# Kernel optimization log

Measured on AMD Instinct MI355X. Metric: run time of the kernel, lower is better.

## Reference

```python
import jax, jax.numpy as jnp
import numpy as np

EPS_IN = 1e-5   # InstanceNorm eps
EPS_L1 = 1e-12  # F.normalize eps


def conv1x1(x, w, b):
    # x: [B,C,H,W], w: [O,C], b: [O]
    return jnp.einsum('bchw,oc->bohw', x, w) + b[None, :, None, None]


def conv3x3_reflect(x, w, b):
    xp = jnp.pad(x, ((0, 0), (0, 0), (1, 1), (1, 1)), mode='reflect')
    y = jax.lax.conv_general_dilated(xp, w, (1, 1), 'VALID',
                                     dimension_numbers=('NCHW', 'OIHW', 'NCHW'))
    return y + b[None, :, None, None]


def instance_norm(x):
    mu = x.mean(axis=(2, 3), keepdims=True)
    var = x.var(axis=(2, 3), keepdims=True)  # biased, matches torch InstanceNorm
    return (x - mu) * jax.lax.rsqrt(var + EPS_IN)


def res_block(x, w1, b1, w2, b2):
    h = jax.nn.relu(instance_norm(conv3x3_reflect(x, w1, b1)))
    h = instance_norm(conv3x3_reflect(h, w2, b2))
    return x + h


def _nearest_idx(out_size, in_size):
    # torch F.interpolate(mode='nearest'): src = floor(dst * in/out)
    return (np.arange(out_size) * in_size) // out_size


def forward(x, mask, g_w, g_b, theta_w, theta_b, phi_w, phi_b, W_w, W_b,
            res_w1, res_b1, res_w2, res_b2):
    B, C, H, Wd = x.shape
    N = H * Wd
    g_x = conv1x1(x, g_w, g_b).reshape(B, -1, N).transpose(0, 2, 1)      # [B,N,Ci]
    theta_x = conv1x1(x, theta_w, theta_b).reshape(B, -1, N).transpose(0, 2, 1)
    phi_x = conv1x1(x, phi_w, phi_b).reshape(B, -1, N)                   # [B,Ci,N]
    f = jnp.einsum('bnc,bcm->bnm', theta_x, phi_x)  # temperature = 1.0
    f_div_C = jax.nn.softmax(f, axis=2)
    # mask pipeline
    m = jax.image.resize(mask, (B, 1, H, Wd), method='linear')  # bilinear, half-pixel (align_corners=False)
    m = jnp.where(m > 0, 1.0, m)
    m = 1.0 - m
    hi = _nearest_idx(H, mask.shape[2])
    wi = _nearest_idx(Wd, mask.shape[3])
    tmp = (1.0 - mask)[:, :, hi][:, :, :, wi]  # nearest upsample of (1-mask)
    m = m * tmp                                 # [B,1,H,W]
    f_div_C = f_div_C * m.reshape(B, 1, N)      # broadcast instead of N^2 repeat
    # re_norm=True: L1 renormalize along keys
    f_div_C = f_div_C / jnp.maximum(jnp.sum(jnp.abs(f_div_C), axis=2, keepdims=True), EPS_L1)
    y = jnp.einsum('bnm,bmc->bnc', f_div_C, g_x)             # [B,N,Ci]
    y = y.transpose(0, 2, 1).reshape(B, -1, H, Wd)
    W_y = conv1x1(y, W_w, W_b)
    for i in range(3):
        W_y = res_block(W_y, res_w1[i], res_b1[i], res_w2[i], res_b2[i])
    z = m * x + (1.0 - m) * W_y
    return z


def setup_inputs() -> dict:
    key = jax.random.key(0)
    ks = jax.random.split(key, 16)
    B, C, H, W = 4, 256, 64, 64
    x = jax.random.normal(ks[0], (B, C, H, W), dtype=jnp.float32)
    mask = (jax.random.uniform(ks[1], (B, 1, 32, 32)) < 0.5).astype(jnp.float32)
    s = 0.02
    d = {
        'x': x, 'mask': mask,
        'g_w': jax.random.normal(ks[2], (C, C), jnp.float32) * s,
        'g_b': jnp.zeros((C,), jnp.float32),
        'theta_w': jax.random.normal(ks[3], (C, C), jnp.float32) * s,
        'theta_b': jnp.zeros((C,), jnp.float32),
        'phi_w': jax.random.normal(ks[4], (C, C), jnp.float32) * s,
        'phi_b': jnp.zeros((C,), jnp.float32),
        'W_w': jax.random.normal(ks[5], (C, C), jnp.float32) * s,
        'W_b': jnp.zeros((C,), jnp.float32),
        'res_w1': jax.random.normal(ks[6], (3, C, C, 3, 3), jnp.float32) * s,
        'res_b1': jnp.zeros((3, C), jnp.float32),
        'res_w2': jax.random.normal(ks[7], (3, C, C, 3, 3), jnp.float32) * s,
        'res_b2': jnp.zeros((3, C), jnp.float32),
    }
    return d


def reference(x, mask, g_w, g_b, theta_w, theta_b, phi_w, phi_b, W_w, W_b,
              res_w1, res_b1, res_w2, res_b2):
    return forward(x, mask, g_w, g_b, theta_w, theta_b, phi_w, phi_b, W_w, W_b,
                   res_w1, res_b1, res_w2, res_b2)
```

## Files before the change

### kernel.cpp

```cpp
#include <hip/hip_runtime.h>

#define BB   4
#define CC   256
#define NPIX 4096
#define PB   1048576
#define NTOT 16384

typedef __attribute__((ext_vector_type(8))) short bf16x8;
typedef __attribute__((ext_vector_type(4))) float f32x4;
typedef __attribute__((ext_vector_type(4))) unsigned short u16x4;

__device__ __forceinline__ unsigned short f2b(float f) {
  union { float f; unsigned u; } v; v.f = f;
  unsigned r = v.u + 0x7fffu + ((v.u >> 16) & 1u);
  return (unsigned short)(r >> 16);
}
__device__ __forceinline__ float b2f(unsigned short h) {
  union { unsigned u; float f; } v; v.u = ((unsigned)h) << 16;
  return v.f;
}
__device__ __forceinline__ f32x4 mfma16(bf16x8 a, bf16x8 b, f32x4 c) {
  return __builtin_amdgcn_mfma_f32_16x16x32_bf16(a, b, c, 0, 0, 0);
}
__device__ __forceinline__ void gload_lds16(const unsigned short* g, unsigned short* l) {
  __builtin_amdgcn_global_load_lds(
      (const __attribute__((address_space(1))) unsigned int*)g,
      (__attribute__((address_space(3))) unsigned int*)l, 16, 0, 0);
}
__device__ __forceinline__ int remap_px(int n, int dh, int dw) {
  int h = (n >> 6) + dh;
  int w = (n & 63) + dw;
  h = h < 0 ? 1 : (h > 63 ? 62 : h);
  w = w < 0 ? 1 : (w > 63 ? 62 : w);
  return (h << 6) | w;
}

__global__ void repack_w1x1_k(const float* __restrict__ tw, const float* __restrict__ pw,
                              const float* __restrict__ gw, const float* __restrict__ Ww,
                              unsigned short* __restrict__ dst) {
  int i = blockIdx.x * 256 + threadIdx.x;
  dst[i]           = f2b(tw[i]);
  dst[65536 + i]   = f2b(pw[i]);
  dst[131072 + i]  = f2b(gw[i]);
  dst[196608 + i]  = f2b(Ww[i]);
}

__global__ void repack_bias_k(const float* __restrict__ tb, const float* __restrict__ pb,
                              const float* __restrict__ gb, const float* __restrict__ Wb,
                              float* __restrict__ bias) {
  int i = blockIdx.x * 256 + threadIdx.x;
  float v;
  if (i < 256) v = tb[i];
  else if (i < 512) v = pb[i - 256];
  else if (i < 768) v = gb[i - 512];
  else v = Wb[i - 768];
  bias[i] = v;
}

__global__ void repack_res_k(const float* __restrict__ w1, const float* __restrict__ w2,
                             unsigned short* __restrict__ wk) {
  int idx = blockIdx.x * 256 + threadIdx.x;
  if (idx >= 1769472) return;
  int t = idx % 9;
  int rest = idx / 9;
  int c = rest & 255;
  int o = (rest >> 8) & 255;
  int i = rest >> 16;
  size_t d = (size_t)t * 65536 + o * 256 + c;
  wk[(size_t)(2 * i)     * 589824 + d] = f2b(w1[idx]);
  wk[(size_t)(2 * i + 1) * 589824 + d] = f2b(w2[idx]);
}

__global__ void prep_mask_k(const float* __restrict__ mask, float* __restrict__ m) {
  int idx = blockIdx.x * 256 + threadIdx.x;
  if (idx >= BB * NPIX) return;
  int b = idx >> 12, n = idx & 4095;
  int h = n >> 6, w = n & 63;
  const float* M = mask + b * 1024;
  float sh = 0.5f * h - 0.25f, sw = 0.5f * w - 0.25f;
  int h0 = (int)floorf(sh), w0 = (int)floorf(sw);
  float th = sh - h0, tw = sw - w0;
  int h0c = min(max(h0, 0), 31), h1c = min(max(h0 + 1, 0), 31);
  int w0c = min(max(w0, 0), 31), w1c = min(max(w0 + 1, 0), 31);
  float v = (1.f - th) * ((1.f - tw) * M[h0c * 32 + w0c] + tw * M[h0c * 32 + w1c])
          +        th  * ((1.f - tw) * M[h1c * 32 + w0c] + tw * M[h1c * 32 + w1c]);
  float inv = v > 0.f ? 0.f : 1.f;
  float tmp = 1.f - M[(h >> 1) * 32 + (w >> 1)];
  m[idx] = inv * tmp;
}

__global__ void mask_scan_k(const float* __restrict__ mbuf, int* __restrict__ ci,
                            int* __restrict__ kcount) {
  int b = blockIdx.x;
  int tid = threadIdx.x;
  __shared__ int sc[256];
  const float* mb = mbuf + b * 4096;
  int n0 = tid * 16, cnt = 0;
  float mv[16];
  #pragma unroll
  for (int i = 0; i < 16; ++i) { mv[i] = mb[n0 + i]; cnt += mv[i] > 0.f ? 1 : 0; }
  sc[tid] = cnt;
  __syncthreads();
  for (int off = 1; off < 256; off <<= 1) {
    int v = sc[tid];
    int u = tid >= off ? sc[tid - off] : 0;
    __syncthreads();
    sc[tid] = v + u;
    __syncthreads();
  }
  int base = sc[tid] - cnt;
  int* cib = ci + b * 4096;
  #pragma unroll
  for (int i = 0; i < 16; ++i)
    if (mv[i] > 0.f) cib[base++] = n0 + i;
  if (tid == 255) kcount[b] = sc[255];
}

__global__ void gather_phi_k(const unsigned short* __restrict__ phb, const int* __restrict__ ci,
                             const int* __restrict__ kcount, unsigned short* __restrict__ phic) {
  int b = blockIdx.y;
  int Kb = kcount[b];
  int pad = (Kb + 63) & ~63;
  int j = blockIdx.x * 8 + (threadIdx.x >> 5);
  int cl = threadIdx.x & 31;
  if (j >= pad) return;
  bf16x8 v;
  if (j < Kb) {
    v = *(const bf16x8*)(phb + (size_t)b * PB + (size_t)ci[b * 4096 + j] * 256 + cl * 8);
  } else {
    for (int t = 0; t < 8; ++t) v[t] = 0;
  }
  *(bf16x8*)(phic + (size_t)b * PB + (size_t)j * 256 + cl * 8) = v;
}

__global__ void gather_g_k(const unsigned short* __restrict__ gbuf, const int* __restrict__ ci,
                           const int* __restrict__ kcount, unsigned short* __restrict__ gc) {
  int b = blockIdx.z;
  int Kb = kcount[b];
  int pad = (Kb + 63) & ~63;
  int c = blockIdx.y;
  int j = blockIdx.x * 256 + threadIdx.x;
  if (j >= pad) return;
  unsigned short v = 0;
  if (j < Kb) v = gbuf[(size_t)c * NTOT + b * 4096 + ci[b * 4096 + j]];
  gc[(size_t)c * NTOT + b * 4096 + j] = v;
}

__global__ void transpose_x_k(const float* __restrict__ x, unsigned short* __restrict__ xT) {
  __shared__ float T[64][65];
  int b = blockIdx.z;
  int n0 = blockIdx.x * 64, c0 = blockIdx.y * 64;
  int tx = threadIdx.x, ty = threadIdx.y;
  const float* xb = x + (size_t)b * PB;
  #pragma unroll
  for (int i = 0; i < 16; ++i) {
    int cl = ty + i * 4;
    T[cl][tx] = xb[(size_t)(c0 + cl) * NPIX + n0 + tx];
  }
  __syncthreads();
  unsigned short* ob = xT + (size_t)b * PB;
  #pragma unroll
  for (int i = 0; i < 16; ++i) {
    int nl = ty + i * 4;
    ob[(size_t)(n0 + nl) * CC + c0 + tx] = f2b(T[tx][nl]);
  }
}

template <int EPI, int TAPS>
__launch_bounds__(256, 2)
__global__ void gemm_w(const unsigned short* __restrict__ A,
                       const unsigned short* __restrict__ Bact,
                       const float* __restrict__ bias,
                       float* __restrict__ outF,
                       unsigned short* __restrict__ o0,
                       unsigned short* __restrict__ o1,
                       unsigned short* __restrict__ o2) {
  int m0 = blockIdx.y * 128;
  int bxs = (blockIdx.x & 7) * 32 + (blockIdx.x >> 3);
  int n0 = bxs * 64;
  int tid = threadIdx.x, lane = tid & 63, wid = tid >> 6;
  int wm = wid >> 1, wn = wid & 1;
  int r16 = lane & 15, g4 = lane >> 4;
  __shared__ __align__(16) unsigned short As[8192];
  __shared__ __align__(16) unsigned short Bs[4096];
  f32x4 acc[4][2] = {};
  int srow[4], scolel[4];
  #pragma unroll
  for (int i = 0; i < 4; ++i) {
    int L = tid * 16 + i * 4096;
    int row = L >> 7;
    srow[i] = row;
    scolel[i] = ((L & 127) ^ ((row & 7) << 4)) >> 1;
  }
  int ra[4], qa[4];
  #pragma unroll
  for (int i = 0; i < 4; ++i) { int r = wm * 64 + i * 16 + r16; ra[i] = r * 128; qa[i] = r & 7; }
  int rbb[2], qb[2];
  #pragma unroll
  for (int j = 0; j < 2; ++j) { int c = wn * 32 + j * 16 + r16; rbb[j] = c * 128; qb[j] = c & 7; }

  const int nsteps = TAPS * 4;
  for (int st = 0; st < nsteps; ++st) {
    int tap = st >> 2;
    int k0 = (st & 3) * 64;
    const unsigned short* At = A + tap * 65536;
    __syncthreads();
    #pragma unroll
    for (int i = 0; i < 4; ++i)
      gload_lds16(At + (size_t)(m0 + srow[i]) * 256 + k0 + scolel[i],
                  &As[(tid * 16 + i * 4096) >> 1]);
    #pragma unroll
    for (int i = 0; i < 2; ++i) {
      int n = n0 + srow[i];
      int bsrc = n;
      if (TAPS == 9) bsrc = (n & ~4095) | remap_px(n & 4095, tap / 3 - 1, tap % 3 - 1);
      gload_lds16(Bact + (size_t)bsrc * 256 + k0 + scolel[i],
                  &Bs[(tid * 16 + i * 4096) >> 1]);
    }
    __syncthreads();
    #pragma unroll
    for (int kk = 0; kk < 2; ++kk) {
      bf16x8 af[4], bfv[2];
      #pragma unroll
      for (int i = 0; i < 4; ++i)
        af[i] = *(const bf16x8*)((const char*)As + ra[i] + (((kk * 4 + g4) ^ qa[i]) << 4));
      #pragma unroll
      for (int j = 0; j < 2; ++j)
        bfv[j] = *(const bf16x8*)((const char*)Bs + rbb[j] + (((kk * 4 + g4) ^ qb[j]) << 4));
      #pragma unroll
      for (int i = 0; i < 4; ++i)
        #pragma unroll
        for (int j = 0; j < 2; ++j)
          acc[i][j] = mfma16(af[i], bfv[j], acc[i][j]);
    }
  }
  #pragma unroll
  for (int i = 0; i < 4; ++i) {
    int row = m0 + wm * 64 + i * 16 + g4 * 4;
    #pragma unroll
    for (int j = 0; j < 2; ++j) {
      int n = n0 + wn * 32 + j * 16 + r16;
      f32x4 v = acc[i][j];
      if constexpr (EPI == 0) {
        int sec = row >> 8;
        int ch = row & 255;
        if (sec < 2) {
          u16x4 pk;
          #pragma unroll
          for (int r = 0; r < 4; ++r) pk[r] = f2b(v[r] + bias[row + r]);
          *(u16x4*)((sec ? o1 : o0) + (size_t)n * 256 + ch) = pk;
        } else {
          #pragma unroll
          for (int r = 0; r < 4; ++r)
            o2[(size_t)(ch + r) * NTOT + n] = f2b(v[r] + bias[row + r]);
        }
      } else if constexpr (EPI == 1) {
        u16x4 pk;
        #pragma unroll
        for (int r = 0; r < 4; ++r) pk[r] = f2b(v[r]);
        *(u16x4*)(o0 + (size_t)n * 256 + row) = pk;
      } else {
        #pragma unroll
        for (int r = 0; r < 4; ++r) v[r] += bias[row + r];
        *(f32x4*)(outF + (size_t)n * 256 + row) = v;
        u16x4 pk;
        #pragma unroll
        for (int r = 0; r < 4; ++r) pk[r] = f2b(v[r]);
        *(u16x4*)(o0 + (size_t)n * 256 + row) = pk;
      }
    }
  }
}

__launch_bounds__(512, 2)
__global__ void attn_k(const unsigned short* __restrict__ theta,
                       const unsigned short* __restrict__ phic,
                       const unsigned short* __restrict__ gc,
                       const int* __restrict__ kcount,
                       float* __restrict__ Op0,
                       float* __restrict__ Op1,
                       float2* __restrict__ ml2) {
  int f = blockIdx.x;
  int b = (f & 7) >> 1;
  int s = f & 1;
  int q0 = (f >> 3) * 128;
  int tid = threadIdx.x, lane = tid & 63, wid = tid >> 6;
  int r16 = lane & 15, g4 = lane >> 4;
  const unsigned short* th = theta + (size_t)b * PB;
  const unsigned short* phb = phic + (size_t)b * PB;

  int Kb = kcount[b];
  int nt = (Kb + 63) >> 6;
  int h = (nt + 1) >> 1;
  int t0 = s * h, t1 = min(nt, t0 + h);

  __shared__ __align__(16) unsigned short Kt[2][16384];
  __shared__ __align__(16) unsigned short Vt[2][16384];
  __shared__ __align__(16) unsigned short Plds[8][16][72];

  int qrow = q0 + wid * 16 + r16;
  bf16x8 aq[8];
  #pragma unroll
  for (int ks = 0; ks < 8; ++ks)
    aq[ks] = *(const bf16x8*)(th + (size_t)qrow * CC + ks * 32 + 8 * g4);

  f32x4 O[16];
  #pragma unroll
  for (int cf = 0; cf < 16; ++cf) { O[cf][0] = 0.f; O[cf][1] = 0.f; O[cf][2] = 0.f; O[cf][3] = 0.f; }
  float mrow[4] = {-1e30f, -1e30f, -1e30f, -1e30f};
  float lrow[4] = {0.f, 0.f, 0.f, 0.f};

  bf16x8 kst[4], vst[4];
  if (t0 < t1) {
    int k0g = t0 * 64;
    #pragma unroll
    for (int i = 0; i < 4; ++i) {
      int slot = wid * 4 + i;
      kst[i] = *(const bf16x8*)(phb + (size_t)(k0g + lane) * CC + slot * 8);
      vst[i] = *(const bf16x8*)(gc + (size_t)(i * 64 + lane) * NTOT + b * 4096 + k0g + wid * 8);
    }
    #pragma unroll
    for (int i = 0; i < 4; ++i) {
      int slot = wid * 4 + i;
      *(bf16x8*)&Kt[0][slot * 512 + lane * 8] = kst[i];
      *(bf16x8*)&Vt[0][wid * 2048 + i * 512 + lane * 8] = vst[i];
    }
  }
  __syncthreads();

  #pragma unroll 1
  for (int t = t0; t < t1; ++t) {
    int p = (t - t0) & 1;
    if (t + 1 < t1) {
      int k0g = (t + 1) * 64;
      #pragma unroll
      for (int i = 0; i < 4; ++i) {
        int slot = wid * 4 + i;
        kst[i] = *(const bf16x8*)(phb + (size_t)(k0g + lane) * CC + slot * 8);
        vst[i] = *(const bf16x8*)(gc + (size_t)(i * 64 + lane) * NTOT + b * 4096 + k0g + wid * 8);
      }
    }
    f32x4 S[4];
    #pragma unroll
    for (int ff = 0; ff < 4; ++ff) { S[ff][0] = 0.f; S[ff][1] = 0.f; S[ff][2] = 0.f; S[ff][3] = 0.f; }
    #pragma unroll
    for (int ks = 0; ks < 8; ++ks) {
      #pragma unroll
      for (int ff = 0; ff < 4; ++ff) {
        bf16x8 bk = *(const bf16x8*)&Kt[p][(ks * 4 + g4) * 512 + (ff * 16 + r16) * 8];
        S[ff] = mfma16(aq[ks], bk, S[ff]);
      }
    }
    bool mk[4];
    #pragma unroll
    for (int ff = 0; ff < 4; ++ff) mk[ff] = (t * 64 + ff * 16 + r16) < Kb;
    float scr[4];
    #pragma unroll
    for (int r = 0; r < 4; ++r) {
      float v = -1e30f;
      #pragma unroll
      for (int ff = 0; ff < 4; ++ff) v = fmaxf(v, mk[ff] ? S[ff][r] : -1e30f);
      v = fmaxf(v, __shfl_xor(v, 1));
      v = fmaxf(v, __shfl_xor(v, 2));
      v = fmaxf(v, __shfl_xor(v, 4));
      v = fmaxf(v, __shfl_xor(v, 8));
      float nm = fmaxf(mrow[r], v);
      scr[r] = __expf(mrow[r] - nm);
      mrow[r] = nm;
      lrow[r] *= scr[r];
    }
    float ps[4][4];
    float rsum[4] = {0.f, 0.f, 0.f, 0.f};
    #pragma unroll
    for (int ff = 0; ff < 4; ++ff)
      #pragma unroll
      for (int r = 0; r < 4; ++r) {
        float pp = mk[ff] ? __expf(S[ff][r] - mrow[r]) : 0.f;
        ps[ff][r] = pp;
        rsum[r] += pp;
      }
    #pragma unroll
    for (int r = 0; r < 4; ++r) {
      float sm = rsum[r];
      sm += __shfl_xor(sm, 1);
      sm += __shfl_xor(sm, 2);
      sm += __shfl_xor(sm, 4);
      sm += __shfl_xor(sm, 8);
      lrow[r] += sm;
    }
    #pragma unroll
    for (int cf = 0; cf < 16; ++cf) {
      O[cf][0] *= scr[0]; O[cf][1] *= scr[1]; O[cf][2] *= scr[2]; O[cf][3] *= scr[3];
    }
    #pragma unroll
    for (int ff = 0; ff < 4; ++ff)
      #pragma unroll
      for (int r = 0; r < 4; ++r)
        Plds[wid][g4 * 4 + r][ff * 16 + r16] = f2b(ps[ff][r]);
    #pragma unroll
    for (int ks2 = 0; ks2 < 2; ++ks2) {
      bf16x8 ap = *(const bf16x8*)&Plds[wid][r16][ks2 * 32 + 8 * g4];
      #pragma unroll
      for (int cf = 0; cf < 16; ++cf) {
        bf16x8 bv = *(const bf16x8*)&Vt[p][(ks2 * 4 + g4) * 2048 + (cf * 16 + r16) * 8];
        O[cf] = mfma16(ap, bv, O[cf]);
      }
    }
    if (t + 1 < t1) {
      #pragma unroll
      for (int i = 0; i < 4; ++i) {
        int slot = wid * 4 + i;
        *(bf16x8*)&Kt[p ^ 1][slot * 512 + lane * 8] = kst[i];
        *(bf16x8*)&Vt[p ^ 1][wid * 2048 + i * 512 + lane * 8] = vst[i];
      }
    }
    __syncthreads();
  }

  float* Opb = (s ? Op1 : Op0) + (size_t)b * NPIX * CC;
  #pragma unroll
  for (int cf = 0; cf < 16; ++cf)
    #pragma unroll
    for (int r = 0; r < 4; ++r)
      Opb[(size_t)(q0 + wid * 16 + g4 * 4 + r) * CC + cf * 16 + r16] = O[cf][r];
  if (r16 == 0) {
    #pragma unroll
    for (int r = 0; r < 4; ++r)
      ml2[(size_t)(s * BB + b) * NPIX + q0 + wid * 16 + g4 * 4 + r] =
          make_float2(mrow[r], lrow[r]);
  }
}

__global__ void attn_combine_k(const float* __restrict__ Op0, const float* __restrict__ Op1,
                               const float2* __restrict__ ml2, unsigned short* __restrict__ y) {
  size_t e = ((size_t)blockIdx.x * 256 + threadIdx.x) * 8;
  int bn = (int)(e >> 8);
  float2 a = ml2[bn];
  float2 c = ml2[16384 + bn];
  float M = fmaxf(a.x, c.x);
  float e0 = __expf(a.x - M), e1 = __expf(c.x - M);
  float L = a.y * e0 + c.y * e1;
  float sc = L > 1e-30f ? 1.f / L : 0.f;
  e0 *= sc; e1 *= sc;
  f32x4 p0 = *(const f32x4*)&Op0[e];
  f32x4 p1 = *(const f32x4*)&Op0[e + 4];
  f32x4 q0 = *(const f32x4*)&Op1[e];
  f32x4 q1 = *(const f32x4*)&Op1[e + 4];
  bf16x8 r;
  #pragma unroll
  for (int j = 0; j < 4; ++j) {
    r[j]     = (short)f2b(p0[j] * e0 + q0[j] * e1);
    r[4 + j] = (short)f2b(p1[j] * e0 + q1[j] * e1);
  }
  *(bf16x8*)&y[e] = r;
}

__global__ void in_stats_k(const unsigned short* __restrict__ v,
                           float* __restrict__ psum, float* __restrict__ psumsq) {
  int p = blockIdx.x;
  int b = blockIdx.y;
  int c = threadIdx.x;
  const unsigned short* base = v + (size_t)b * PB + (size_t)p * 128 * CC + c;
  float s = 0.f, s2 = 0.f;
  for (int n = 0; n < 128; ++n) {
    float f = b2f(base[n * CC]);
    s += f; s2 += f * f;
  }
  int o = (p * BB + b) * CC + c;
  psum[o] = s; psumsq[o] = s2;
}

__global__ void in_finalize_k(const float* __restrict__ psum, const float* __restrict__ psumsq,
                              float* __restrict__ mu, float* __restrict__ rs) {
  int bc = blockIdx.x * 256 + threadIdx.x;
  int b = bc >> 8, c = bc & 255;
  float s = 0.f, s2 = 0.f;
  for (int p = 0; p < 32; ++p) {
    s  += psum[(p * BB + b) * CC + c];
    s2 += psumsq[(p * BB + b) * CC + c];
  }
  float m_ = s * (1.f / 4096.f);
  float var = s2 * (1.f / 4096.f) - m_ * m_;
  var = var > 0.f ? var : 0.f;
  mu[bc] = m_;
  rs[bc] = rsqrtf(var + 1e-5f);
}

__global__ void normrelu_k(const unsigned short* __restrict__ src,
                           const float* __restrict__ mu, const float* __restrict__ rs,
                           unsigned short* __restrict__ dst) {
  size_t idx = (size_t)blockIdx.x * 256 + threadIdx.x;
  size_t e = idx * 8;
  if (e >= (size_t)BB * PB) return;
  int c = (int)(e & 255);
  int b = (int)(e >> 20);
  const float* mup = mu + b * 256 + c;
  const float* rsp = rs + b * 256 + c;
  bf16x8 v = *(const bf16x8*)(src + e);
  bf16x8 ov;
  #pragma unroll
  for (int j = 0; j < 8; ++j) {
    float f = (b2f((unsigned short)v[j]) - mup[j]) * rsp[j];
    ov[j] = (short)f2b(f > 0.f ? f : 0.f);
  }
  *(bf16x8*)(dst + e) = ov;
}

__global__ void resupdate_k(const unsigned short* __restrict__ c2,
                            const float* __restrict__ mu, const float* __restrict__ rs,
                            float* __restrict__ r, unsigned short* __restrict__ rb) {
  size_t idx = (size_t)blockIdx.x * 256 + threadIdx.x;
  size_t e = idx * 8;
  if (e >= (size_t)BB * PB) return;
  int c = (int)(e & 255);
  int b = (int)(e >> 20);
  const float* mup = mu + b * 256 + c;
  const float* rsp = rs + b * 256 + c;
  bf16x8 v = *(const bf16x8*)(c2 + e);
  bf16x8 ov;
  #pragma unroll
  for (int j = 0; j < 8; ++j) {
    float f = r[e + j] + (b2f((unsigned short)v[j]) - mup[j]) * rsp[j];
    r[e + j] = f;
    ov[j] = (short)f2b(f);
  }
  *(bf16x8*)(rb + e) = ov;
}

__global__ void final_blend_k(const float* __restrict__ x, const float* __restrict__ r,
                              const float* __restrict__ m, float* __restrict__ out) {
  __shared__ float T[64][65];
  int b = blockIdx.z;
  int n0 = blockIdx.x * 64, c0 = blockIdx.y * 64;
  int tx = threadIdx.x, ty = threadIdx.y;
  #pragma unroll
  for (int i = 0; i < 16; ++i) {
    int nl = ty + i * 4;
    T[nl][tx] = r[(size_t)b * PB + (size_t)(n0 + nl) * CC + c0 + tx];
  }
  __syncthreads();
  #pragma unroll
  for (int i = 0; i < 16; ++i) {
    int cl = ty + i * 4;
    int cg = c0 + cl, ng = n0 + tx;
    float mv = m[b * NPIX + ng];
    float xv = x[(size_t)b * PB + (size_t)cg * NPIX + ng];
    out[(size_t)b * PB + (size_t)cg * NPIX + ng] = mv * xv + (1.f - mv) * T[tx][cl];
  }
}

#define OFF_M    0UL
#define OFF_XT   65536UL
#define OFF_TH   8454144UL
#define OFF_PH   16842752UL
#define OFF_G    25231360UL
#define OFF_R    33619968UL
#define OFF_W1   50397184UL
#define OFF_WK   50921472UL
#define OFF_MU   57999360UL
#define OFF_RS   58003456UL
#define OFF_PS   58007552UL
#define OFF_PS2  58138624UL
#define OFF_OP1  58269696UL
#define OFF_ML   75046912UL
#define OFF_CI   75309056UL
#define OFF_KC   75374592UL
#define OFF_BIAS 75374848UL

extern "C" void kernel_launch(void* const* d_in, const int* in_sizes, int n_in,
                              void* d_out, int out_size, void* d_ws, size_t ws_size,
                              hipStream_t stream) {
  const float* x       = (const float*)d_in[0];
  const float* maskp   = (const float*)d_in[1];
  const float* g_w     = (const float*)d_in[2];
  const float* g_b     = (const float*)d_in[3];
  const float* theta_w = (const float*)d_in[4];
  const float* theta_b = (const float*)d_in[5];
  const float* phi_w   = (const float*)d_in[6];
  const float* phi_b   = (const float*)d_in[7];
  const float* W_w     = (const float*)d_in[8];
  const float* W_b     = (const float*)d_in[9];
  const float* res_w1  = (const float*)d_in[10];
  const float* res_w2  = (const float*)d_in[12];
  float* out = (float*)d_out;
  char* ws = (char*)d_ws;

  float*          mbuf = (float*)(ws + OFF_M);
  unsigned short* xT   = (unsigned short*)(ws + OFF_XT);
  unsigned short* phic = (unsigned short*)(ws + OFF_XT);
  unsigned short* ybuf = (unsigned short*)(ws + OFF_XT);
  unsigned short* thb  = (unsigned short*)(ws + OFF_TH);
  unsigned short* cbuf = (unsigned short*)(ws + OFF_TH);
  unsigned short* phb  = (unsigned short*)(ws + OFF_PH);
  unsigned short* gc   = (unsigned short*)(ws + OFF_PH);
  unsigned short* hbuf = (unsigned short*)(ws + OFF_PH);
  unsigned short* gbuf = (unsigned short*)(ws + OFF_G);
  unsigned short* rb   = (unsigned short*)(ws + OFF_G);
  float*          rbuf = (float*)(ws + OFF_R);
  float*          op0  = (float*)(ws + OFF_R);
  float*          op1  = (float*)(ws + OFF_OP1);
  float2*         ml2  = (float2*)(ws + OFF_ML);
  int*            ci   = (int*)(ws + OFF_CI);
  int*            kc   = (int*)(ws + OFF_KC);
  float*          biasS= (float*)(ws + OFF_BIAS);
  unsigned short* thw  = (unsigned short*)(ws + OFF_W1);
  unsigned short* Www  = (unsigned short*)(ws + OFF_W1 + 393216);
  unsigned short* wkres= (unsigned short*)(ws + OFF_WK);
  float*          mu   = (float*)(ws + OFF_MU);
  float*          rs   = (float*)(ws + OFF_RS);
  float*          psum = (float*)(ws + OFF_PS);
  float*          psq  = (float*)(ws + OFF_PS2);

  repack_w1x1_k<<<256, 256, 0, stream>>>(theta_w, phi_w, g_w, W_w, thw);
  repack_res_k<<<6912, 256, 0, stream>>>(res_w1, res_w2, wkres);
  repack_bias_k<<<4, 256, 0, stream>>>(theta_b, phi_b, g_b, W_b, biasS);
  prep_mask_k<<<64, 256, 0, stream>>>(maskp, mbuf);
  transpose_x_k<<<dim3(64, 4, 4), dim3(64, 4), 0, stream>>>(x, xT);

  gemm_w<0, 1><<<dim3(256, 6), 256, 0, stream>>>(thw, xT, biasS, nullptr, thb, phb, gbuf);

  mask_scan_k<<<4, 256, 0, stream>>>(mbuf, ci, kc);
  gather_phi_k<<<dim3(512, 4), 256, 0, stream>>>(phb, ci, kc, phic);
  gather_g_k<<<dim3(16, 256, 4), 256, 0, stream>>>(gbuf, ci, kc, gc);

  attn_k<<<256, 512, 0, stream>>>(thb, phic, gc, kc, op0, op1, ml2);
  attn_combine_k<<<2048, 256, 0, stream>>>(op0, op1, ml2, ybuf);

  gemm_w<2, 1><<<dim3(256, 2), 256, 0, stream>>>(Www, ybuf, biasS + 768, rbuf, rb, nullptr, nullptr);

  for (int i = 0; i < 3; ++i) {
    gemm_w<1, 9><<<dim3(256, 2), 256, 0, stream>>>(
        wkres + (size_t)(2 * i) * 589824, rb, nullptr, nullptr, cbuf, nullptr, nullptr);
    in_stats_k<<<dim3(32, 4), 256, 0, stream>>>(cbuf, psum, psq);
    in_finalize_k<<<4, 256, 0, stream>>>(psum, psq, mu, rs);
    normrelu_k<<<2048, 256, 0, stream>>>(cbuf, mu, rs, hbuf);
    gemm_w<1, 9><<<dim3(256, 2), 256, 0, stream>>>(
        wkres + (size_t)(2 * i + 1) * 589824, hbuf, nullptr, nullptr, cbuf, nullptr, nullptr);
    in_stats_k<<<dim3(32, 4), 256, 0, stream>>>(cbuf, psum, psq);
    in_finalize_k<<<4, 256, 0, stream>>>(psum, psq, mu, rs);
    resupdate_k<<<2048, 256, 0, stream>>>(cbuf, mu, rs, rbuf, rb);
  }

  final_blend_k<<<dim3(64, 4, 4), dim3(64, 4), 0, stream>>>(x, rbuf, mbuf, out);
}
```

Measured before the change: 515.6 us.

## Double-buffer GEMM LDS tiles with 2-wave blocks and vectorize instance-norm stats

The shared GEMM kernel moves to 128-thread blocks. Each wave now computes a 64x64 tile with 4x4 MFMA accumulators, and A/B tiles are double-buffered in LDS so the next k-step's global-to-LDS loads overlap the current MFMAs, with one barrier per step instead of two. Separately, the instance-norm stats kernel now reads 8 bf16 channels per thread as a vector load and reduces across row groups in shared memory, replacing strided scalar loads. The GEMM change doubles LDS per block and raises accumulator register pressure. Fewer waves per block may reduce latency hiding.

```diff
diff --git a/kernel.cpp b/kernel.cpp
--- a/kernel.cpp
+++ b/kernel.cpp
@@ -167,7 +167,7 @@
 }
 
 template <int EPI, int TAPS>
-__launch_bounds__(256, 2)
+__launch_bounds__(128, 2)
 __global__ void gemm_w(const unsigned short* __restrict__ A,
                        const unsigned short* __restrict__ Bact,
                        const float* __restrict__ bias,
@@ -179,67 +179,77 @@
   int bxs = (blockIdx.x & 7) * 32 + (blockIdx.x >> 3);
   int n0 = bxs * 64;
   int tid = threadIdx.x, lane = tid & 63, wid = tid >> 6;
-  int wm = wid >> 1, wn = wid & 1;
   int r16 = lane & 15, g4 = lane >> 4;
-  __shared__ __align__(16) unsigned short As[8192];
-  __shared__ __align__(16) unsigned short Bs[4096];
-  f32x4 acc[4][2] = {};
-  int srow[4], scolel[4];
+  __shared__ __align__(16) unsigned short As[2 * 8192];
+  __shared__ __align__(16) unsigned short Bs[2 * 4096];
+  f32x4 acc[4][4] = {};
+  int sr[8], sc[8];
+  #pragma unroll
+  for (int q = 0; q < 8; ++q) {
+    sr[q] = (tid >> 3) + q * 16;
+    sc[q] = (((tid * 16) & 127) ^ ((sr[q] & 7) << 4)) >> 1;
+  }
+  int q7 = r16 & 7;
+  int ra[4], rbv[4];
+  #pragma unroll
+  for (int i = 0; i < 4; ++i) ra[i] = (wid * 64 + i * 16 + r16) * 128;
+  #pragma unroll
+  for (int j = 0; j < 4; ++j) rbv[j] = (j * 16 + r16) * 128;
+
+  const int nsteps = TAPS * 4;
+
+#define STAGE(st_, bs_) do {                                                      \
+    int tap_ = (st_) >> 2, k0_ = ((st_) & 3) * 64;                                \
+    const unsigned short* At_ = A + tap_ * 65536;                                 \
+    _Pragma("unroll")                                                             \
+    for (int q = 0; q < 8; ++q)                                                   \
+      gload_lds16(At_ + (size_t)(m0 + sr[q]) * 256 + k0_ + sc[q],                 \
+                  &As[(bs_) * 8192 + tid * 8 + q * 1024]);                        \
+    _Pragma("unroll")                                                             \
+    for (int q = 0; q < 4; ++q) {                                                 \
+      int n_ = n0 + sr[q];                                                        \
+      int bsrc_ = n_;                                                             \
+      if (TAPS == 9) bsrc_ = (n_ & ~4095) | remap_px(n_ & 4095, tap_ / 3 - 1, tap_ % 3 - 1); \
+      gload_lds16(Bact + (size_t)bsrc_ * 256 + k0_ + sc[q],                       \
+                  &Bs[(bs_) * 4096 + tid * 8 + q * 1024]);                        \
+    }                                                                             \
+  } while (0)
+
+#define COMPUTE(bs_) do {                                                         \
+    _Pragma("unroll")                                                             \
+    for (int kk = 0; kk < 2; ++kk) {                                              \
+      bf16x8 af_[4], bf_[4];                                                      \
+      _Pragma("unroll")                                                           \
+      for (int i = 0; i < 4; ++i)                                                 \
+        af_[i] = *(const bf16x8*)((const char*)As + (bs_) * 16384 + ra[i] +       \
+                                  (((kk * 4 + g4) ^ q7) << 4));                   \
+      _Pragma("unroll")                                                           \
+      for (int j = 0; j < 4; ++j)                                                 \
+        bf_[j] = *(const bf16x8*)((const char*)Bs + (bs_) * 8192 + rbv[j] +       \
+                                  (((kk * 4 + g4) ^ q7) << 4));                   \
+      _Pragma("unroll")                                                           \
+      for (int i = 0; i < 4; ++i)                                                 \
+        _Pragma("unroll")                                                         \
+        for (int j = 0; j < 4; ++j)                                               \
+          acc[i][j] = mfma16(af_[i], bf_[j], acc[i][j]);                          \
+    }                                                                             \
+  } while (0)
+
+  STAGE(0, 0);
+  for (int st = 0; st < nsteps; ++st) {
+    __syncthreads();
+    if (st + 1 < nsteps) STAGE(st + 1, (st + 1) & 1);
+    COMPUTE(st & 1);
+  }
+#undef STAGE
+#undef COMPUTE
+
   #pragma unroll
   for (int i = 0; i < 4; ++i) {
-    int L = tid * 16 + i * 4096;
-    int row = L >> 7;
-    srow[i] = row;
-    scolel[i] = ((L & 127) ^ ((row & 7) << 4)) >> 1;
-  }
-  int ra[4], qa[4];
-  #pragma unroll
-  for (int i = 0; i < 4; ++i) { int r = wm * 64 + i * 16 + r16; ra[i] = r * 128; qa[i] = r & 7; }
-  int rbb[2], qb[2];
-  #pragma unroll
-  for (int j = 0; j < 2; ++j) { int c = wn * 32 + j * 16 + r16; rbb[j] = c * 128; qb[j] = c & 7; }
-
-  const int nsteps = TAPS * 4;
-  for (int st = 0; st < nsteps; ++st) {
-    int tap = st >> 2;
-    int k0 = (st & 3) * 64;
-    const unsigned short* At = A + tap * 65536;
-    __syncthreads();
-    #pragma unroll
-    for (int i = 0; i < 4; ++i)
-      gload_lds16(At + (size_t)(m0 + srow[i]) * 256 + k0 + scolel[i],
-                  &As[(tid * 16 + i * 4096) >> 1]);
-    #pragma unroll
-    for (int i = 0; i < 2; ++i) {
-      int n = n0 + srow[i];
-      int bsrc = n;
-      if (TAPS == 9) bsrc = (n & ~4095) | remap_px(n & 4095, tap / 3 - 1, tap % 3 - 1);
-      gload_lds16(Bact + (size_t)bsrc * 256 + k0 + scolel[i],
-                  &Bs[(tid * 16 + i * 4096) >> 1]);
-    }
-    __syncthreads();
-    #pragma unroll
-    for (int kk = 0; kk < 2; ++kk) {
-      bf16x8 af[4], bfv[2];
-      #pragma unroll
-      for (int i = 0; i < 4; ++i)
-        af[i] = *(const bf16x8*)((const char*)As + ra[i] + (((kk * 4 + g4) ^ qa[i]) << 4));
-      #pragma unroll
-      for (int j = 0; j < 2; ++j)
-        bfv[j] = *(const bf16x8*)((const char*)Bs + rbb[j] + (((kk * 4 + g4) ^ qb[j]) << 4));
-      #pragma unroll
-      for (int i = 0; i < 4; ++i)
-        #pragma unroll
-        for (int j = 0; j < 2; ++j)
-          acc[i][j] = mfma16(af[i], bfv[j], acc[i][j]);
-    }
-  }
-  #pragma unroll
-  for (int i = 0; i < 4; ++i) {
-    int row = m0 + wm * 64 + i * 16 + g4 * 4;
-    #pragma unroll
-    for (int j = 0; j < 2; ++j) {
-      int n = n0 + wn * 32 + j * 16 + r16;
+    int row = m0 + wid * 64 + i * 16 + g4 * 4;
+    #pragma unroll
+    for (int j = 0; j < 4; ++j) {
+      int n = n0 + j * 16 + r16;
       f32x4 v = acc[i][j];
       if constexpr (EPI == 0) {
         int sec = row >> 8;
@@ -459,15 +469,30 @@
                            float* __restrict__ psum, float* __restrict__ psumsq) {
   int p = blockIdx.x;
   int b = blockIdx.y;
-  int c = threadIdx.x;
-  const unsigned short* base = v + (size_t)b * PB + (size_t)p * 128 * CC + c;
-  float s = 0.f, s2 = 0.f;
-  for (int n = 0; n < 128; ++n) {
-    float f = b2f(base[n * CC]);
-    s += f; s2 += f * f;
-  }
-  int o = (p * BB + b) * CC + c;
-  psum[o] = s; psumsq[o] = s2;
+  int tid = threadIdx.x;
+  int cg = (tid & 31) * 8;
+  int rsub = tid >> 5;
+  const unsigned short* base = v + (size_t)b * PB + (size_t)p * 128 * CC;
+  float s[8] = {}, s2[8] = {};
+  for (int it = 0; it < 16; ++it) {
+    int row = rsub + it * 8;
+    bf16x8 x = *(const bf16x8*)(base + (size_t)row * CC + cg);
+    #pragma unroll
+    for (int j = 0; j < 8; ++j) {
+      float f = b2f((unsigned short)x[j]);
+      s[j] += f; s2[j] += f * f;
+    }
+  }
+  __shared__ float redS[8][256];
+  __shared__ float redQ[8][256];
+  #pragma unroll
+  for (int j = 0; j < 8; ++j) { redS[rsub][cg + j] = s[j]; redQ[rsub][cg + j] = s2[j]; }
+  __syncthreads();
+  float a = 0.f, q = 0.f;
+  #pragma unroll
+  for (int r = 0; r < 8; ++r) { a += redS[r][tid]; q += redQ[r][tid]; }
+  int o = (p * BB + b) * CC + tid;
+  psum[o] = a; psumsq[o] = q;
 }
 
 __global__ void in_finalize_k(const float* __restrict__ psum, const float* __restrict__ psumsq,
@@ -617,7 +642,7 @@
   prep_mask_k<<<64, 256, 0, stream>>>(maskp, mbuf);
   transpose_x_k<<<dim3(64, 4, 4), dim3(64, 4), 0, stream>>>(x, xT);
 
-  gemm_w<0, 1><<<dim3(256, 6), 256, 0, stream>>>(thw, xT, biasS, nullptr, thb, phb, gbuf);
+  gemm_w<0, 1><<<dim3(256, 6), 128, 0, stream>>>(thw, xT, biasS, nullptr, thb, phb, gbuf);
 
   mask_scan_k<<<4, 256, 0, stream>>>(mbuf, ci, kc);
   gather_phi_k<<<dim3(512, 4), 256, 0, stream>>>(phb, ci, kc, phic);
@@ -626,15 +651,15 @@
   attn_k<<<256, 512, 0, stream>>>(thb, phic, gc, kc, op0, op1, ml2);
   attn_combine_k<<<2048, 256, 0, stream>>>(op0, op1, ml2, ybuf);
 
-  gemm_w<2, 1><<<dim3(256, 2), 256, 0, stream>>>(Www, ybuf, biasS + 768, rbuf, rb, nullptr, nullptr);
+  gemm_w<2, 1><<<dim3(256, 2), 128, 0, stream>>>(Www, ybuf, biasS + 768, rbuf, rb, nullptr, nullptr);
 
   for (int i = 0; i < 3; ++i) {
-    gemm_w<1, 9><<<dim3(256, 2), 256, 0, stream>>>(
+    gemm_w<1, 9><<<dim3(256, 2), 128, 0, stream>>>(
         wkres + (size_t)(2 * i) * 589824, rb, nullptr, nullptr, cbuf, nullptr, nullptr);
     in_stats_k<<<dim3(32, 4), 256, 0, stream>>>(cbuf, psum, psq);
     in_finalize_k<<<4, 256, 0, stream>>>(psum, psq, mu, rs);
     normrelu_k<<<2048, 256, 0, stream>>>(cbuf, mu, rs, hbuf);
-    gemm_w<1, 9><<<dim3(256, 2), 256, 0, stream>>>(
+    gemm_w<1, 9><<<dim3(256, 2), 128, 0, stream>>>(
         wkres + (size_t)(2 * i + 1) * 589824, hbuf, nullptr, nullptr, cbuf, nullptr, nullptr);
     in_stats_k<<<dim3(32, 4), 256, 0, stream>>>(cbuf, psum, psq);
     in_finalize_k<<<4, 256, 0, stream>>>(psum, psq, mu, rs);
```

Result: slower. 589.6 us (+14.4%).
